# Kernel tuning notes

Measured on AMD Instinct MI355X. Metric: run time of the kernel, lower is better.

## Reference

```python
import jax, jax.numpy as jnp
import numpy as np

N_NODES = 100000
N_EDGES = 1600000
D = 64          # in_channels = hidden_channels = out_channels
L = 3           # num_layers


def setup_inputs() -> dict:
    key = jax.random.key(0)
    ks = jax.random.split(key, 10)
    s = 0.05
    x = jax.random.normal(ks[0], (N_NODES, D), dtype=jnp.float32)
    edge_index = jax.random.randint(ks[1], (2, N_EDGES), 0, N_NODES, dtype=jnp.int32)
    # stacked per-layer GIN MLP params (all layers are D->D since in==hidden)
    W1 = jax.random.normal(ks[2], (L, D, D), dtype=jnp.float32) * s
    b1 = jnp.zeros((L, D), dtype=jnp.float32)
    W2 = jax.random.normal(ks[3], (L, D, D), dtype=jnp.float32) * s
    b2 = jnp.zeros((L, D), dtype=jnp.float32)
    eps = jnp.zeros((L,), dtype=jnp.float32)  # train_eps=True, init 0
    Wf = jax.random.normal(ks[4], (D, D), dtype=jnp.float32) * s
    bf = jnp.zeros((D,), dtype=jnp.float32)
    return {"x": x, "edge_index": edge_index, "W1": W1, "b1": b1,
            "W2": W2, "b2": b2, "eps": eps, "Wf": Wf, "bf": bf}


def reference(x, edge_index, W1, b1, W2, b2, eps, Wf, bf):
    n = x.shape[0]
    src, dst = edge_index[0], edge_index[1]
    for l in range(L):
        # GINConv: out = MLP((1+eps)*x + sum_{j in N(i)} x_j)
        agg = jax.ops.segment_sum(x[src], dst, num_segments=n)  # [N, D]
        h = (1.0 + eps[l]) * x + agg
        h = jax.nn.relu(h @ W1[l] + b1[l])
        x = jax.nn.relu(h @ W2[l] + b2[l])
    return x @ Wf + bf
```

## Files before the change

kernel.cpp:

```cpp
#include <hip/hip_runtime.h>

#define NN 100000
#define NE 1600000
#define DIM 64
#define NR 391
#define BP 400
#define MH (NR * BP)
#define NSB2 611
#define IDXCAP 1664
#define DUMMY (64u << 17)

typedef unsigned short u16;
typedef unsigned int u32;
typedef __attribute__((ext_vector_type(8))) short short8;
typedef __attribute__((ext_vector_type(4))) float f32x4;

__device__ __forceinline__ u16 f2b(float f) {
  union { float f; u32 u; } c; c.f = f;
  u32 u = c.u;
  u += 0x7FFF + ((u >> 16) & 1);
  return (u16)(u >> 16);
}
__device__ __forceinline__ float blo(u32 v) {
  union { u32 u; float f; } c; c.u = v << 16;
  return c.f;
}
__device__ __forceinline__ float bhi(u32 v) {
  union { u32 u; float f; } c; c.u = v & 0xFFFF0000u;
  return c.f;
}
__device__ __forceinline__ u32 pk(float lo, float hi) {
  return ((u32)f2b(hi) << 16) | (u32)f2b(lo);
}

union FragU { u32 w[4]; short8 v; };

__global__ __launch_bounds__(256) void k_tobf(const float* __restrict__ x,
                                              u16* __restrict__ xh) {
  int i = blockIdx.x * 256 + threadIdx.x;
  float4 v = ((const float4*)x)[i];
  ushort4 o;
  o.x = f2b(v.x); o.y = f2b(v.y); o.z = f2b(v.z); o.w = f2b(v.w);
  ((ushort4*)xh)[i] = o;
}

__global__ __launch_bounds__(256) void k_wconv(const float* __restrict__ W1,
                                               const float* __restrict__ W2,
                                               const float* __restrict__ Wf,
                                               u32* __restrict__ wt) {
  int m = blockIdx.x;
  const float* src = (m < 3) ? (W1 + m * 4096) : (m < 6 ? (W2 + (m - 3) * 4096) : Wf);
  for (int c = threadIdx.x; c < 2048; c += 256) {
    int j = c >> 5, kk = c & 31;
    wt[m * 2048 + c] = pk(src[(2 * kk) * 64 + j], src[(2 * kk + 1) * 64 + j]);
  }
}


__global__ __launch_bounds__(256) void k_phist(const int* __restrict__ ei,
                                               int* __restrict__ Hmat) {
  __shared__ int lh[NR];
  const int t = threadIdx.x;
  const int b = blockIdx.x;
  for (int i = t; i < NR; i += 256) lh[i] = 0;
  __syncthreads();
  const int e0 = b * 4000;
  for (int k = 0; k < 16; ++k) {
    int o = k * 256 + t;
    if (o < 4000) atomicAdd(&lh[ei[NE + e0 + o] >> 8], 1);
  }
  __syncthreads();
  for (int i = t; i < NR; i += 256) Hmat[i * BP + b] = lh[i];
}

__global__ __launch_bounds__(256) void k_sA(int* __restrict__ a,
                                            int* __restrict__ bsum) {
  __shared__ int buf[256];
  const int t = threadIdx.x;
  const int i = blockIdx.x * 256 + t;
  int v = (i < MH) ? a[i] : 0;
  buf[t] = v;
  __syncthreads();
  for (int off = 1; off < 256; off <<= 1) {
    int u = (t >= off) ? buf[t - off] : 0;
    __syncthreads();
    buf[t] += u;
    __syncthreads();
  }
  if (i < MH) a[i] = buf[t] - v;
  if (t == 255) bsum[blockIdx.x] = buf[255];
}

__global__ __launch_bounds__(1024) void k_sB(int* __restrict__ bsum) {
  __shared__ int buf[1024];
  const int t = threadIdx.x;
  int v = (t < NSB2) ? bsum[t] : 0;
  buf[t] = v;
  __syncthreads();
  for (int off = 1; off < 1024; off <<= 1) {
    int u = (t >= off) ? buf[t - off] : 0;
    __syncthreads();
    buf[t] += u;
    __syncthreads();
  }
  if (t < NSB2) bsum[t] = buf[t] - v;
}

__global__ __launch_bounds__(256) void k_sC(int* __restrict__ a,
                                            const int* __restrict__ bsum) {
  int i = blockIdx.x * 256 + threadIdx.x;
  if (i < MH) a[i] += bsum[blockIdx.x];
}

__global__ __launch_bounds__(512) void k_rex(const int* __restrict__ Hs,
                                             int* __restrict__ rstart,
                                             int* __restrict__ nstartP) {
  int t = threadIdx.x;
  if (t < NR) rstart[t] = Hs[t * BP];
  if (t == 0) { rstart[NR] = NE; nstartP[NN] = NE; }
}

__global__ __launch_bounds__(256) void k_pfill(const int* __restrict__ ei,
                                               const int* __restrict__ Hs,
                                               int* __restrict__ bb) {
  __shared__ int lcur[NR];
  const int t = threadIdx.x;
  const int b = blockIdx.x;
  for (int i = t; i < NR; i += 256) lcur[i] = Hs[i * BP + b];
  __syncthreads();
  const int e0 = b * 4000;
  for (int k = 0; k < 16; ++k) {
    int o = k * 256 + t;
    if (o < 4000) {
      int e = e0 + o;
      int src = ei[e];
      int dst = ei[NE + e];
      int p = atomicAdd(&lcur[dst >> 8], 1);
      bb[p] = src | ((dst & 255) << 17);
    }
  }
}

__global__ __launch_bounds__(256) void k_rsort(const int* __restrict__ rstart,
                                               const int* __restrict__ bb,
                                               int* __restrict__ csr2,
                                               int* __restrict__ nstartP) {
  __shared__ int nhist[256], ncur[256], buf[256];
  const int t = threadIdx.x;
  const int r = blockIdx.x;
  const int s = rstart[r];
  const int cnt = rstart[r + 1] - s;
  const int nb = r << 8;
  nhist[t] = 0;
  __syncthreads();
  for (int p = t; p < cnt; p += 256) atomicAdd(&nhist[bb[s + p] >> 17], 1);
  __syncthreads();
  int v = nhist[t];
  buf[t] = v;
  __syncthreads();
  for (int off = 1; off < 256; off <<= 1) {
    int u = (t >= off) ? buf[t - off] : 0;
    __syncthreads();
    buf[t] += u;
    __syncthreads();
  }
  int st = s + buf[t] - v;
  ncur[t] = st;
  if (nb + t < NN) nstartP[nb + t] = st;
  __syncthreads();
  for (int p = t; p < cnt; p += 256) {
    int e2 = bb[s + p];
    int loc = e2 >> 17;
    int pos = atomicAdd(&ncur[loc], 1);
    csr2[pos] = (e2 & 0x1FFFF) | ((loc & 63) << 17);
  }
}

__device__ __forceinline__ void mfma_gemm(const u32* T32, const u32* __restrict__ wt,
                                          int wvv, int lr, int lg, f32x4 acc[4]) {
  FragU a0, a1;
  const int abase = (16 * wvv + lr) * 33 + 4 * lg;
#pragma unroll
  for (int c = 0; c < 4; ++c) { a0.w[c] = T32[abase + c]; a1.w[c] = T32[abase + 16 + c]; }
#pragma unroll
  for (int t = 0; t < 4; ++t) {
    FragU b0, b1;
    const u32* wp = wt + (16 * t + lr) * 32 + 4 * lg;
#pragma unroll
    for (int c = 0; c < 4; ++c) { b0.w[c] = wp[c]; b1.w[c] = wp[16 + c]; }
    acc[t] = __builtin_amdgcn_mfma_f32_16x16x32_bf16(a0.v, b0.v, acc[t], 0, 0, 0);
    acc[t] = __builtin_amdgcn_mfma_f32_16x16x32_bf16(a1.v, b1.v, acc[t], 0, 0, 0);
  }
}

__device__ __forceinline__ void pack_relu(u32* T32, int wvv, int lr, int lg,
                                          const f32x4 acc[4]) {
#pragma unroll
  for (int t = 0; t < 4; ++t)
#pragma unroll
    for (int r = 0; r < 4; ++r) {
      float v = fmaxf(acc[t][r], 0.0f);
      float p = __shfl_xor(v, 1, 64);
      if ((lr & 1) == 0)
        T32[(16 * wvv + 4 * lg + r) * 33 + 8 * t + (lr >> 1)] = pk(v, p);
    }
}

#define LOADCHUNK(EV, VV, P0)                              \
  _Pragma("unroll")                                        \
  for (int i_ = 0; i_ < 16; ++i_) {                        \
    int p_ = (P0) + i_;                                    \
    EV[i_] = (p_ < ge) ? (u32)sidx[p_] : DUMMY;            \
  }                                                        \
  _Pragma("unroll")                                        \
  for (int i_ = 0; i_ < 16; ++i_)                          \
    VV[i_] = xu[(size_t)(EV[i_] & 0x1FFFF) * 32 + fl];

#define FLUSH(CUR)                                          \
  {                                                         \
    float s0_ = 0.f, s1_ = 0.f;                             \
    if ((CUR) < rows) {                                     \
      u32 su_ = xu[(size_t)(base + (CUR)) * 32 + fl];       \
      s0_ = sc * blo(su_); s1_ = sc * bhi(su_);             \
    }                                                       \
    tile32[(CUR) * 33 + fl] = pk(s0_ + a0, s1_ + a1);       \
  }

#define PROCCHUNK(EV, VV)                                  \
  _Pragma("unroll")                                        \
  for (int i_ = 0; i_ < 16; ++i_) {                        \
    int n_ = (int)(EV[i_] >> 17);                          \
    if (n_ != cur) {                                       \
      FLUSH(cur)                                           \
      cur = n_; a0 = 0.f; a1 = 0.f;                        \
    }                                                      \
    a0 += blo(VV[i_]); a1 += bhi(VV[i_]);                  \
  }

template <int FINAL>
__global__ __launch_bounds__(256, 8) void k_gin(const u16* __restrict__ xh,
                                                const int* __restrict__ nstartP,
                                                const int* __restrict__ csr2,
                                                const float* __restrict__ eps, int l,
                                                const u32* __restrict__ wt1,
                                                const float* __restrict__ b1,
                                                const u32* __restrict__ wt2,
                                                const float* __restrict__ b2,
                                                u16* __restrict__ outh,
                                                const u32* __restrict__ wtf,
                                                const float* __restrict__ bf,
                                                float* __restrict__ outf) {
  __shared__ u32 tile32[65 * 33];
  __shared__ int sidx[IDXCAP];
  __shared__ int sstart[9];
  const int tid = threadIdx.x;
  const int lane = tid & 63;
  const int wvv = tid >> 6;
  const int h = lane >> 5;
  const int fl = lane & 31;
  const int base = blockIdx.x * 64;
  const int rows = min(64, NN - base);
  const float sc = 1.0f + eps[l];
  const u32* xu = (const u32*)xh;

  const int s0 = nstartP[base];
  const int cnt = nstartP[min(base + 64, NN)] - s0;
  if (tid < 9) sstart[tid] = nstartP[min(base + 8 * tid, NN)];
  const bool fast = (cnt <= IDXCAP);

#pragma unroll
  for (int c = 0; c < 8; ++c) {
    int row = 16 * wvv + 2 * c + h;
    u32 w = 0;
    if (row < rows) {
      u32 u_ = xu[(size_t)(base + row) * 32 + fl];
      w = pk(sc * blo(u_), sc * bhi(u_));
    }
    tile32[row * 33 + fl] = w;
  }
  if (fast)
    for (int p = tid; p < cnt; p += 256) sidx[p] = csr2[s0 + p];
  __syncthreads();

  const int hw = wvv * 2 + h;
  const int gs = sstart[hw] - s0;
  const int ge = sstart[hw + 1] - s0;
  int cur = 64;
  float a0 = 0.f, a1 = 0.f;
  if (fast) {
    for (int p0 = gs; p0 < ge; p0 += 16) {
      u32 ev[16], v[16];
      LOADCHUNK(ev, v, p0)
      PROCCHUNK(ev, v)
    }
  } else {
    for (int p0 = gs; p0 < ge; p0 += 16) {
#pragma unroll
      for (int i = 0; i < 16; ++i) {
        int p = p0 + i;
        u32 ev = (p < ge) ? (u32)csr2[s0 + p] : DUMMY;
        u32 vv = xu[(size_t)(ev & 0x1FFFF) * 32 + fl];
        int n = (int)(ev >> 17);
        if (n != cur) {
          FLUSH(cur)
          cur = n; a0 = 0.f; a1 = 0.f;
        }
        a0 += blo(vv); a1 += bhi(vv);
      }
    }
  }
  FLUSH(cur)

  const int lr = lane & 15;
  const int lg = lane >> 4;
  f32x4 acc[4];

#pragma unroll
  for (int t = 0; t < 4; ++t) {
    float bv = b1[16 * t + lr];
    acc[t] = (f32x4){bv, bv, bv, bv};
  }
  mfma_gemm(tile32, wt1, wvv, lr, lg, acc);
  pack_relu(tile32, wvv, lr, lg, acc);

#pragma unroll
  for (int t = 0; t < 4; ++t) {
    float bv = b2[16 * t + lr];
    acc[t] = (f32x4){bv, bv, bv, bv};
  }
  mfma_gemm(tile32, wt2, wvv, lr, lg, acc);
  pack_relu(tile32, wvv, lr, lg, acc);

  if constexpr (FINAL == 0) {
    u32* o32 = (u32*)outh;
#pragma unroll
    for (int rr = 0; rr < 8; ++rr) {
      int row = 16 * wvv + 2 * rr + h;
      if (row < rows) o32[(size_t)(base + row) * 32 + fl] = tile32[row * 33 + fl];
    }
  } else {
#pragma unroll
    for (int t = 0; t < 4; ++t) {
      float bv = bf[16 * t + lr];
      acc[t] = (f32x4){bv, bv, bv, bv};
    }
    mfma_gemm(tile32, wtf, wvv, lr, lg, acc);
#pragma unroll
    for (int t = 0; t < 4; ++t)
#pragma unroll
      for (int r = 0; r < 4; ++r) {
        int row = 16 * wvv + 4 * lg + r;
        if (row < rows) outf[(size_t)(base + row) * 64 + 16 * t + lr] = acc[t][r];
      }
  }
}

extern "C" void kernel_launch(void* const* d_in, const int* in_sizes, int n_in,
                              void* d_out, int out_size, void* d_ws, size_t ws_size,
                              hipStream_t stream) {
  const float* x   = (const float*)d_in[0];
  const int*   ei  = (const int*)d_in[1];
  const float* W1  = (const float*)d_in[2];
  const float* b1  = (const float*)d_in[3];
  const float* W2  = (const float*)d_in[4];
  const float* b2  = (const float*)d_in[5];
  const float* eps = (const float*)d_in[6];
  const float* Wf  = (const float*)d_in[7];
  const float* bf  = (const float*)d_in[8];

  u16* xh0 = (u16*)d_ws;
  u16* xh1 = xh0 + (size_t)NN * DIM;
  int* csr2    = (int*)(xh1 + (size_t)NN * DIM);
  int* nstartP = csr2 + NE;
  int* Hmat    = nstartP + NN + 1;
  int* bsum    = Hmat + MH;
  int* rstart  = bsum + NSB2;
  u32* wt      = (u32*)(rstart + NR + 1);
  int* bb = (int*)d_out;

  const int grid_conv = NN * DIM / 4 / 256;
  const int grid_mlp  = (NN + 63) / 64;

  k_tobf<<<grid_conv, 256, 0, stream>>>(x, xh0);
  k_wconv<<<7, 256, 0, stream>>>(W1, W2, Wf, wt);
  k_phist<<<BP, 256, 0, stream>>>(ei, Hmat);
  k_sA<<<NSB2, 256, 0, stream>>>(Hmat, bsum);
  k_sB<<<1, 1024, 0, stream>>>(bsum);
  k_sC<<<NSB2, 256, 0, stream>>>(Hmat, bsum);
  k_rex<<<1, 512, 0, stream>>>(Hmat, rstart, nstartP);
  k_pfill<<<BP, 256, 0, stream>>>(ei, Hmat, bb);
  k_rsort<<<NR, 256, 0, stream>>>(rstart, bb, csr2, nstartP);

  k_gin<0><<<grid_mlp, 256, 0, stream>>>(xh0, nstartP, csr2, eps, 0,
                                         wt + 0 * 2048, b1, wt + 3 * 2048, b2,
                                         xh1, wt + 6 * 2048, bf, nullptr);
  k_gin<0><<<grid_mlp, 256, 0, stream>>>(xh1, nstartP, csr2, eps, 1,
                                         wt + 1 * 2048, b1 + 64, wt + 4 * 2048, b2 + 64,
                                         xh0, wt + 6 * 2048, bf, nullptr);
  k_gin<1><<<grid_mlp, 256, 0, stream>>>(xh0, nstartP, csr2, eps, 2,
                                         wt + 2 * 2048, b1 + 128, wt + 5 * 2048, b2 + 128,
                                         xh1, wt + 6 * 2048, bf, (float*)d_out);
}
```

Measured before the change: 205.4 us.

## Gather neighbor rows with 8-byte loads over quarter-wave groups and prescaled byte offsets

Each neighbor row is now gathered by 16 lanes issuing 8-byte loads, where before 32 lanes issued 4-byte loads, so a wave handles four node groups of 4 rows each. The CSR entries are re-encoded to store the source index pre-shifted as a byte offset (index<<7) with the local destination in the top bits. This saves the address multiply and shortens per-edge work. The aim is fewer memory instructions per gathered row and more independent gathers in flight. In exchange, chunks shrink from 16 to 8 edges, each lane keeps more accumulators, and source indices must fit in 18 bits.

```diff
diff --git a/kernel.cpp b/kernel.cpp
--- a/kernel.cpp
+++ b/kernel.cpp
@@ -8,7 +8,7 @@
 #define MH (NR * BP)
 #define NSB2 611
 #define IDXCAP 1664
-#define DUMMY (64u << 17)
+#define DUMMY (64u << 25)
 
 typedef unsigned short u16;
 typedef unsigned int u32;
@@ -172,7 +172,7 @@
     int e2 = bb[s + p];
     int loc = e2 >> 17;
     int pos = atomicAdd(&ncur[loc], 1);
-    csr2[pos] = (e2 & 0x1FFFF) | ((loc & 63) << 17);
+    csr2[pos] = (int)(((u32)(e2 & 0x1FFFF) << 7) | ((u32)(loc & 63) << 25));
   }
 }
 
@@ -206,35 +206,38 @@
     }
 }
 
-#define LOADCHUNK(EV, VV, P0)                              \
+#define FLUSHQ(CUR)                                            \
+  {                                                            \
+    float s0_ = 0.f, s1_ = 0.f, s2_ = 0.f, s3_ = 0.f;          \
+    if ((CUR) < rows) {                                        \
+      uint2 su_ = *(const uint2*)(xsb + (CUR) * 128);          \
+      s0_ = sc * blo(su_.x); s1_ = sc * bhi(su_.x);            \
+      s2_ = sc * blo(su_.y); s3_ = sc * bhi(su_.y);            \
+    }                                                          \
+    tile32[(CUR) * 33 + 2 * ql]     = pk(s0_ + a0, s1_ + a1);  \
+    tile32[(CUR) * 33 + 2 * ql + 1] = pk(s2_ + a2, s3_ + a3);  \
+  }
+
+#define LOADCHUNK8(EV, VV, P0)                             \
   _Pragma("unroll")                                        \
-  for (int i_ = 0; i_ < 16; ++i_) {                        \
+  for (int i_ = 0; i_ < 8; ++i_) {                         \
     int p_ = (P0) + i_;                                    \
     EV[i_] = (p_ < ge) ? (u32)sidx[p_] : DUMMY;            \
   }                                                        \
   _Pragma("unroll")                                        \
-  for (int i_ = 0; i_ < 16; ++i_)                          \
-    VV[i_] = xu[(size_t)(EV[i_] & 0x1FFFF) * 32 + fl];
-
-#define FLUSH(CUR)                                          \
-  {                                                         \
-    float s0_ = 0.f, s1_ = 0.f;                             \
-    if ((CUR) < rows) {                                     \
-      u32 su_ = xu[(size_t)(base + (CUR)) * 32 + fl];       \
-      s0_ = sc * blo(su_); s1_ = sc * bhi(su_);             \
-    }                                                       \
-    tile32[(CUR) * 33 + fl] = pk(s0_ + a0, s1_ + a1);       \
-  }
-
-#define PROCCHUNK(EV, VV)                                  \
+  for (int i_ = 0; i_ < 8; ++i_)                           \
+    VV[i_] = *(const uint2*)(xgb + (EV[i_] & 0x00FFFF80u));
+
+#define PROCCHUNK8(EV, VV)                                 \
   _Pragma("unroll")                                        \
-  for (int i_ = 0; i_ < 16; ++i_) {                        \
-    int n_ = (int)(EV[i_] >> 17);                          \
+  for (int i_ = 0; i_ < 8; ++i_) {                         \
+    int n_ = (int)(EV[i_] >> 25);                          \
     if (n_ != cur) {                                       \
-      FLUSH(cur)                                           \
-      cur = n_; a0 = 0.f; a1 = 0.f;                        \
+      FLUSHQ(cur)                                          \
+      cur = n_; a0 = 0.f; a1 = 0.f; a2 = 0.f; a3 = 0.f;    \
     }                                                      \
-    a0 += blo(VV[i_]); a1 += bhi(VV[i_]);                  \
+    a0 += blo(VV[i_].x); a1 += bhi(VV[i_].x);              \
+    a2 += blo(VV[i_].y); a3 += bhi(VV[i_].y);              \
   }
 
 template <int FINAL>
@@ -252,20 +255,23 @@
                                                 float* __restrict__ outf) {
   __shared__ u32 tile32[65 * 33];
   __shared__ int sidx[IDXCAP];
-  __shared__ int sstart[9];
+  __shared__ int sstart[17];
   const int tid = threadIdx.x;
   const int lane = tid & 63;
   const int wvv = tid >> 6;
   const int h = lane >> 5;
   const int fl = lane & 31;
+  const int ql = lane & 15;
   const int base = blockIdx.x * 64;
   const int rows = min(64, NN - base);
   const float sc = 1.0f + eps[l];
   const u32* xu = (const u32*)xh;
+  const char* xgb = (const char*)xh + ql * 8;
+  const char* xsb = (const char*)xh + (size_t)base * 128 + ql * 8;
 
   const int s0 = nstartP[base];
   const int cnt = nstartP[min(base + 64, NN)] - s0;
-  if (tid < 9) sstart[tid] = nstartP[min(base + 8 * tid, NN)];
+  if (tid < 17) sstart[tid] = nstartP[min(base + 4 * tid, NN)];
   const bool fast = (cnt <= IDXCAP);
 
 #pragma unroll
@@ -282,34 +288,35 @@
     for (int p = tid; p < cnt; p += 256) sidx[p] = csr2[s0 + p];
   __syncthreads();
 
-  const int hw = wvv * 2 + h;
-  const int gs = sstart[hw] - s0;
-  const int ge = sstart[hw + 1] - s0;
+  const int qq = 4 * wvv + (lane >> 4);
+  const int gs = sstart[qq] - s0;
+  const int ge = sstart[qq + 1] - s0;
   int cur = 64;
-  float a0 = 0.f, a1 = 0.f;
+  float a0 = 0.f, a1 = 0.f, a2 = 0.f, a3 = 0.f;
   if (fast) {
-    for (int p0 = gs; p0 < ge; p0 += 16) {
-      u32 ev[16], v[16];
-      LOADCHUNK(ev, v, p0)
-      PROCCHUNK(ev, v)
+    for (int p0 = gs; p0 < ge; p0 += 8) {
+      u32 ev[8]; uint2 v[8];
+      LOADCHUNK8(ev, v, p0)
+      PROCCHUNK8(ev, v)
     }
   } else {
-    for (int p0 = gs; p0 < ge; p0 += 16) {
-#pragma unroll
-      for (int i = 0; i < 16; ++i) {
+    for (int p0 = gs; p0 < ge; p0 += 8) {
+#pragma unroll
+      for (int i = 0; i < 8; ++i) {
         int p = p0 + i;
         u32 ev = (p < ge) ? (u32)csr2[s0 + p] : DUMMY;
-        u32 vv = xu[(size_t)(ev & 0x1FFFF) * 32 + fl];
-        int n = (int)(ev >> 17);
+        uint2 vv = *(const uint2*)(xgb + (ev & 0x00FFFF80u));
+        int n = (int)(ev >> 25);
         if (n != cur) {
-          FLUSH(cur)
-          cur = n; a0 = 0.f; a1 = 0.f;
+          FLUSHQ(cur)
+          cur = n; a0 = 0.f; a1 = 0.f; a2 = 0.f; a3 = 0.f;
         }
-        a0 += blo(vv); a1 += bhi(vv);
+        a0 += blo(vv.x); a1 += bhi(vv.x);
+        a2 += blo(vv.y); a3 += bhi(vv.y);
       }
     }
   }
-  FLUSH(cur)
+  FLUSHQ(cur)
 
   const int lr = lane & 15;
   const int lg = lane >> 4;
```

Result: slower. 213.0 us (+3.7%).

## Shrink GIN node tile from 64 to 48 rows per block

Applied to the files above, without the earlier changes.

Each block of the fused GIN layer kernel now handles 48 nodes instead of 64, and the grid grows to 2084 blocks. The CSR row tag is recomputed modulo 48 so it matches the new tiling. Each of the eight half-waves now aggregates 6 nodes instead of 8, which shortens the per-block gather and reduces shared memory use. Only three of the four waves run the MFMA MLP stage, and an extra barrier is added before it. The intent is better load balance and occupancy for the gather phase, at the cost of an idle wave during the GEMMs and more blocks.

```diff
diff --git a/kernel.cpp b/kernel.cpp
--- a/kernel.cpp
+++ b/kernel.cpp
@@ -7,8 +7,10 @@
 #define BP 400
 #define MH (NR * BP)
 #define NSB2 611
-#define IDXCAP 1664
-#define DUMMY (64u << 17)
+#define TROWS 48
+#define NTIL 2084
+#define IDXCAP 1280
+#define DUMMY (48u << 17)
 
 typedef unsigned short u16;
 typedef unsigned int u32;
@@ -171,8 +173,10 @@
   for (int p = t; p < cnt; p += 256) {
     int e2 = bb[s + p];
     int loc = e2 >> 17;
+    u32 g = (u32)(nb + loc);
+    u32 tag = g - 48u * (g / 48u);
     int pos = atomicAdd(&ncur[loc], 1);
-    csr2[pos] = (e2 & 0x1FFFF) | ((loc & 63) << 17);
+    csr2[pos] = (e2 & 0x1FFFF) | ((int)tag << 17);
   }
 }
 
@@ -250,7 +254,7 @@
                                                 const u32* __restrict__ wtf,
                                                 const float* __restrict__ bf,
                                                 float* __restrict__ outf) {
-  __shared__ u32 tile32[65 * 33];
+  __shared__ u32 tile32[49 * 33];
   __shared__ int sidx[IDXCAP];
   __shared__ int sstart[9];
   const int tid = threadIdx.x;
@@ -258,34 +262,35 @@
   const int wvv = tid >> 6;
   const int h = lane >> 5;
   const int fl = lane & 31;
-  const int base = blockIdx.x * 64;
-  const int rows = min(64, NN - base);
+  const int base = blockIdx.x * TROWS;
+  const int rows = min(TROWS, NN - base);
   const float sc = 1.0f + eps[l];
   const u32* xu = (const u32*)xh;
 
   const int s0 = nstartP[base];
-  const int cnt = nstartP[min(base + 64, NN)] - s0;
-  if (tid < 9) sstart[tid] = nstartP[min(base + 8 * tid, NN)];
+  const int cnt = nstartP[min(base + TROWS, NN)] - s0;
+  if (tid < 9) sstart[tid] = nstartP[min(base + 6 * tid, NN)];
   const bool fast = (cnt <= IDXCAP);
 
 #pragma unroll
-  for (int c = 0; c < 8; ++c) {
-    int row = 16 * wvv + 2 * c + h;
+  for (int c = 0; c < 6; ++c) {
+    int cell = c * 256 + tid;
+    int row = cell >> 5, f = cell & 31;
     u32 w = 0;
     if (row < rows) {
-      u32 u_ = xu[(size_t)(base + row) * 32 + fl];
+      u32 u_ = xu[(size_t)(base + row) * 32 + f];
       w = pk(sc * blo(u_), sc * bhi(u_));
     }
-    tile32[row * 33 + fl] = w;
+    tile32[row * 33 + f] = w;
   }
   if (fast)
     for (int p = tid; p < cnt; p += 256) sidx[p] = csr2[s0 + p];
   __syncthreads();
 
-  const int hw = wvv * 2 + h;
+  const int hw = tid >> 5;
   const int gs = sstart[hw] - s0;
   const int ge = sstart[hw + 1] - s0;
-  int cur = 64;
+  int cur = TROWS;
   float a0 = 0.f, a1 = 0.f;
   if (fast) {
     for (int p0 = gs; p0 < ge; p0 += 16) {
@@ -310,48 +315,50 @@
     }
   }
   FLUSH(cur)
+  __syncthreads();
 
   const int lr = lane & 15;
   const int lg = lane >> 4;
   f32x4 acc[4];
-
-#pragma unroll
-  for (int t = 0; t < 4; ++t) {
-    float bv = b1[16 * t + lr];
-    acc[t] = (f32x4){bv, bv, bv, bv};
-  }
-  mfma_gemm(tile32, wt1, wvv, lr, lg, acc);
-  pack_relu(tile32, wvv, lr, lg, acc);
-
-#pragma unroll
-  for (int t = 0; t < 4; ++t) {
-    float bv = b2[16 * t + lr];
-    acc[t] = (f32x4){bv, bv, bv, bv};
-  }
-  mfma_gemm(tile32, wt2, wvv, lr, lg, acc);
-  pack_relu(tile32, wvv, lr, lg, acc);
-
-  if constexpr (FINAL == 0) {
-    u32* o32 = (u32*)outh;
-#pragma unroll
-    for (int rr = 0; rr < 8; ++rr) {
-      int row = 16 * wvv + 2 * rr + h;
-      if (row < rows) o32[(size_t)(base + row) * 32 + fl] = tile32[row * 33 + fl];
-    }
-  } else {
+  if (wvv < 3) {
 #pragma unroll
     for (int t = 0; t < 4; ++t) {
-      float bv = bf[16 * t + lr];
+      float bv = b1[16 * t + lr];
       acc[t] = (f32x4){bv, bv, bv, bv};
     }
-    mfma_gemm(tile32, wtf, wvv, lr, lg, acc);
-#pragma unroll
-    for (int t = 0; t < 4; ++t)
-#pragma unroll
-      for (int r = 0; r < 4; ++r) {
-        int row = 16 * wvv + 4 * lg + r;
-        if (row < rows) outf[(size_t)(base + row) * 64 + 16 * t + lr] = acc[t][r];
+    mfma_gemm(tile32, wt1, wvv, lr, lg, acc);
+    pack_relu(tile32, wvv, lr, lg, acc);
+
+#pragma unroll
+    for (int t = 0; t < 4; ++t) {
+      float bv = b2[16 * t + lr];
+      acc[t] = (f32x4){bv, bv, bv, bv};
+    }
+    mfma_gemm(tile32, wt2, wvv, lr, lg, acc);
+    pack_relu(tile32, wvv, lr, lg, acc);
+
+    if constexpr (FINAL == 0) {
+      u32* o32 = (u32*)outh;
+#pragma unroll
+      for (int rr = 0; rr < 8; ++rr) {
+        int row = 16 * wvv + 2 * rr + h;
+        if (row < rows) o32[(size_t)(base + row) * 32 + fl] = tile32[row * 33 + fl];
       }
+    } else {
+#pragma unroll
+      for (int t = 0; t < 4; ++t) {
+        float bv = bf[16 * t + lr];
+        acc[t] = (f32x4){bv, bv, bv, bv};
+      }
+      mfma_gemm(tile32, wtf, wvv, lr, lg, acc);
+#pragma unroll
+      for (int t = 0; t < 4; ++t)
+#pragma unroll
+        for (int r = 0; r < 4; ++r) {
+          int row = 16 * wvv + 4 * lg + r;
+          if (row < rows) outf[(size_t)(base + row) * 64 + 16 * t + lr] = acc[t][r];
+        }
+    }
   }
 }
 
@@ -379,7 +386,6 @@
   int* bb = (int*)d_out;
 
   const int grid_conv = NN * DIM / 4 / 256;
-  const int grid_mlp  = (NN + 63) / 64;
 
   k_tobf<<<grid_conv, 256, 0, stream>>>(x, xh0);
   k_wconv<<<7, 256, 0, stream>>>(W1, W2, Wf, wt);
@@ -391,13 +397,13 @@
   k_pfill<<<BP, 256, 0, stream>>>(ei, Hmat, bb);
   k_rsort<<<NR, 256, 0, stream>>>(rstart, bb, csr2, nstartP);
 
-  k_gin<0><<<grid_mlp, 256, 0, stream>>>(xh0, nstartP, csr2, eps, 0,
-                                         wt + 0 * 2048, b1, wt + 3 * 2048, b2,
-                                         xh1, wt + 6 * 2048, bf, nullptr);
-  k_gin<0><<<grid_mlp, 256, 0, stream>>>(xh1, nstartP, csr2, eps, 1,
-                                         wt + 1 * 2048, b1 + 64, wt + 4 * 2048, b2 + 64,
-                                         xh0, wt + 6 * 2048, bf, nullptr);
-  k_gin<1><<<grid_mlp, 256, 0, stream>>>(xh0, nstartP, csr2, eps, 2,
-                                         wt + 2 * 2048, b1 + 128, wt + 5 * 2048, b2 + 128,
-                                         xh1, wt + 6 * 2048, bf, (float*)d_out);
-}
+  k_gin<0><<<NTIL, 256, 0, stream>>>(xh0, nstartP, csr2, eps, 0,
+                                     wt + 0 * 2048, b1, wt + 3 * 2048, b2,
+                                     xh1, wt + 6 * 2048, bf, nullptr);
+  k_gin<0><<<NTIL, 256, 0, stream>>>(xh1, nstartP, csr2, eps, 1,
+                                     wt + 1 * 2048, b1 + 64, wt + 4 * 2048, b2 + 64,
+                                     xh0, wt + 6 * 2048, bf, nullptr);
+  k_gin<1><<<NTIL, 256, 0, stream>>>(xh0, nstartP, csr2, eps, 2,
+                                     wt + 2 * 2048, b1 + 128, wt + 5 * 2048, b2 + 128,
+                                     xh1, wt + 6 * 2048, bf, (float*)d_out);
+}
```

After: 220.3 us. +7.2%, slower.
